# Kernel tuning notes

Hardware: AMD Instinct MI355X
Metric: run time of the kernel (lower is better)

Reference implementation:

```python
import jax, jax.numpy as jnp
import numpy as np

EPS = 1e-8
K = 3  # num_neighbors

def setup_inputs() -> dict:
    key = jax.random.key(0)
    k1, k2, k3, k4 = jax.random.split(key, 4)
    n, B, m, C = 16384, 8, 2048, 128
    return {
        "unknown": jax.random.normal(k1, (n, 3), dtype=jnp.float32),
        "known": jax.random.normal(k2, (B, m, 3), dtype=jnp.float32),
        "batch_inds": jax.random.randint(k3, (n,), 0, B),
        "known_feats": jax.random.normal(k4, (B, C, m), dtype=jnp.float32),
    }

def reference(unknown, known, batch_inds, known_feats):
    # unknown: (n,3); known: (B,m,3); batch_inds: (n,); known_feats: (B,C,m)
    kg = known[batch_inds]                                   # (n,m,3) gather per-query scene
    d2 = jnp.sum((unknown[:, None, :] - kg) ** 2, axis=-1)   # (n,m) squared L2
    neg_d2, idx = jax.lax.top_k(-d2, K)                      # 3 nearest (sorted ascending dist)
    dist = jnp.sqrt(jnp.maximum(-neg_d2, 0.0))               # (n,K)
    dist_recip = 1.0 / (dist + EPS)
    weight = dist_recip / jnp.sum(dist_recip, axis=-1, keepdims=True)  # (n,K)
    # gather neighbor features: (n,K,C)
    feats = known_feats[batch_inds[:, None], :, idx]
    out = jnp.einsum('nkc,nk->nc', feats, weight)            # (n,C)
    return out[:, :, None]                                   # (n,C,1)
```

## Files before the change

kernel.cpp:

```cpp
#include <hip/hip_runtime.h>

#define NPTS 16384
#define NB   8
#define NM   2048
#define NC   128
#define EPSF 1e-8f

#define TQ   16
#define QPB  16
#define GX   160

#define MERGE_F(d, j) do {                              \
    const bool _b2 = (d) < D2;                          \
    const bool _b1 = (d) < D1;                          \
    const bool _b0 = (d) < D0;                          \
    D2 = _b1 ? D1 : (_b2 ? (d) : D2);                   \
    I2 = _b1 ? I1 : (_b2 ? (j) : I2);                   \
    D1 = _b0 ? D0 : (_b1 ? (d) : D1);                   \
    I1 = _b0 ? I0 : (_b1 ? (j) : I1);                   \
    D0 = _b0 ? (d) : D0;                                \
    I0 = _b0 ? (j) : I0;                                \
} while (0)

#define MERGE_DI(ed, ei) do {                                           \
    const bool _b2 = ((ed) < D2) || (((ed) == D2) && ((ei) < I2));      \
    const bool _b1 = ((ed) < D1) || (((ed) == D1) && ((ei) < I1));      \
    const bool _b0 = ((ed) < D0) || (((ed) == D0) && ((ei) < I0));      \
    D2 = _b1 ? D1 : (_b2 ? (ed) : D2);                                  \
    I2 = _b1 ? I1 : (_b2 ? (ei) : I2);                                  \
    D1 = _b0 ? D0 : (_b1 ? (ed) : D1);                                  \
    I1 = _b0 ? I0 : (_b1 ? (ei) : I1);                                  \
    D0 = _b0 ? (ed) : D0;                                               \
    I0 = _b0 ? (ei) : I0;                                               \
} while (0)

__global__ __launch_bounds__(256, 5) void fused(const float* __restrict__ unknown,
                                                const float* __restrict__ known,
                                                const int*   __restrict__ binds,
                                                const float* __restrict__ feats,
                                                float* __restrict__ out) {
    __shared__ float2 kxy[NM];
    __shared__ float  kz[NM];
    __shared__ int qlist[QPB];
    __shared__ int wsum[4];

    const int tid  = threadIdx.x;
    const int b    = blockIdx.y;
    const int x    = blockIdx.x;
    const int lane = tid & 63;
    const int wave = tid >> 6;

    const int4* b4 = (const int4*)binds;
    int myCnt = 0;
#pragma unroll
    for (int r = 0; r < 16; ++r) {
        const int4 v = b4[tid * 16 + r];
        myCnt += (v.x == b) + (v.y == b) + (v.z == b) + (v.w == b);
    }
    int inc = myCnt;
#pragma unroll
    for (int off = 1; off <= 32; off <<= 1) {
        const int n = __shfl_up(inc, off);
        if (lane >= off) inc += n;
    }
    if (lane == 63) wsum[wave] = inc;
    __syncthreads();
    int wbase = 0;
    for (int w = 0; w < wave; ++w) wbase += wsum[w];
    const int exPre = wbase + inc - myCnt;
    const int segN  = wsum[0] + wsum[1] + wsum[2] + wsum[3];

    if (x * QPB >= segN) return;

    {
        const float* kb = known + (size_t)b * NM * 3;
        for (int j = tid; j < NM; j += 256) {
            float2 xy; xy.x = kb[j * 3 + 0]; xy.y = kb[j * 3 + 1];
            kxy[j] = xy;
            kz[j]  = kb[j * 3 + 2];
        }
    }

    const int qi = tid >> 4;
    const int t  = tid & 15;

    for (int w0 = x * QPB; w0 < segN; w0 += GX * QPB) {
        __syncthreads();
        if (exPre < w0 + QPB && exPre + myCnt > w0) {
            int rank = exPre;
#pragma unroll
            for (int r = 0; r < 16; ++r) {
                const int4 v = b4[tid * 16 + r];
                const int base = tid * 64 + r * 4;
                if (v.x == b) { if (rank >= w0 && rank < w0 + QPB) qlist[rank - w0] = base + 0; ++rank; }
                if (v.y == b) { if (rank >= w0 && rank < w0 + QPB) qlist[rank - w0] = base + 1; ++rank; }
                if (v.z == b) { if (rank >= w0 && rank < w0 + QPB) qlist[rank - w0] = base + 2; ++rank; }
                if (v.w == b) { if (rank >= w0 && rank < w0 + QPB) qlist[rank - w0] = base + 3; ++rank; }
            }
        }
        __syncthreads();

        const int valid = (segN - w0 < QPB) ? (segN - w0) : QPB;
        const int kq    = (qi < valid) ? qi : 0;
        const int p     = qlist[kq];
        const float ux = unknown[p * 3 + 0];
        const float uy = unknown[p * 3 + 1];
        const float uz = unknown[p * 3 + 2];

        float D0 = __builtin_inff(), D1 = __builtin_inff(), D2 = __builtin_inff();
        int   I0 = NM, I1 = NM, I2 = NM;

#pragma unroll 8
        for (int i = 0; i < NM / TQ; ++i) {
            const int j = (i << 4) | t;
            const float2 kp = kxy[j];
            const float  kzz = kz[j];
            const float dx = __fsub_rn(ux, kp.x);
            const float dy = __fsub_rn(uy, kp.y);
            const float dz = __fsub_rn(uz, kzz);
            const float d  = __fadd_rn(__fadd_rn(__fmul_rn(dx, dx), __fmul_rn(dy, dy)),
                                       __fmul_rn(dz, dz));
            MERGE_F(d, j);
        }

#pragma unroll
        for (int off = 8; off >= 1; off >>= 1) {
            const float e0d = __shfl_down(D0, off);
            const float e1d = __shfl_down(D1, off);
            const float e2d = __shfl_down(D2, off);
            const int   e0i = __shfl_down(I0, off);
            const int   e1i = __shfl_down(I1, off);
            const int   e2i = __shfl_down(I2, off);
            MERGE_DI(e0d, e0i);
            MERGE_DI(e1d, e1i);
            MERGE_DI(e2d, e2i);
        }
        const int src = lane & ~15;
        D0 = __shfl(D0, src); D1 = __shfl(D1, src); D2 = __shfl(D2, src);
        I0 = __shfl(I0, src); I1 = __shfl(I1, src); I2 = __shfl(I2, src);

        const float t0 = 1.0f / (sqrtf(D0) + EPSF);
        const float t1 = 1.0f / (sqrtf(D1) + EPSF);
        const float t2 = 1.0f / (sqrtf(D2) + EPSF);
        const float s  = t0 + t1 + t2;
        const float w0w = t0 / s, w1w = t1 / s, w2w = t2 / s;

        const float* fb = feats + (size_t)b * NC * NM;
#pragma unroll
        for (int k = 0; k < 8; ++k) {
            const int c = t + (k << 4);
            const float* fc = fb + (size_t)c * NM;
            const float f0 = fc[I0];
            const float f1 = fc[I1];
            const float f2 = fc[I2];
            out[(size_t)p * NC + c] = w0w * f0 + w1w * f1 + w2w * f2;
        }
    }
}

extern "C" void kernel_launch(void* const* d_in, const int* in_sizes, int n_in,
                              void* d_out, int out_size, void* d_ws, size_t ws_size,
                              hipStream_t stream) {
    const float* unknown = (const float*)d_in[0];
    const float* known   = (const float*)d_in[1];
    const int*   binds   = (const int*)d_in[2];
    const float* feats   = (const float*)d_in[3];
    float*       out     = (float*)d_out;

    fused<<<dim3(GX, NB), 256, 0, stream>>>(unknown, known, binds, feats, out);
}
```

Measured before the change: 113.7 us.

## Pack known points as SoA float2 pairs and use med3-based top-3 merge

```diff
diff --git a/kernel.cpp b/kernel.cpp
--- a/kernel.cpp
+++ b/kernel.cpp
@@ -10,16 +10,17 @@
 #define QPB  16
 #define GX   160
 
-#define MERGE_F(d, j) do {                              \
-    const bool _b2 = (d) < D2;                          \
-    const bool _b1 = (d) < D1;                          \
-    const bool _b0 = (d) < D0;                          \
-    D2 = _b1 ? D1 : (_b2 ? (d) : D2);                   \
-    I2 = _b1 ? I1 : (_b2 ? (j) : I2);                   \
-    D1 = _b0 ? D0 : (_b1 ? (d) : D1);                   \
-    I1 = _b0 ? I0 : (_b1 ? (j) : I1);                   \
-    D0 = _b0 ? (d) : D0;                                \
-    I0 = _b0 ? (j) : I0;                                \
+#define MERGE3(d, j) do {                                       \
+    const bool _b0 = (d) < D0;                                  \
+    const bool _b1 = (d) < D1;                                  \
+    const bool _b2 = (d) < D2;                                  \
+    const float _n0 = fminf((d), D0);                           \
+    const float _n1 = __builtin_amdgcn_fmed3f(D0, D1, (d));     \
+    const float _n2 = __builtin_amdgcn_fmed3f(D1, D2, (d));     \
+    I2 = _b1 ? I1 : (_b2 ? (j) : I2);                           \
+    I1 = _b0 ? I0 : (_b1 ? (j) : I1);                           \
+    I0 = _b0 ? (j) : I0;                                        \
+    D0 = _n0; D1 = _n1; D2 = _n2;                               \
 } while (0)
 
 #define MERGE_DI(ed, ei) do {                                           \
@@ -34,13 +35,14 @@
     I0 = _b0 ? (ei) : I0;                                               \
 } while (0)
 
-__global__ __launch_bounds__(256, 5) void fused(const float* __restrict__ unknown,
+__global__ __launch_bounds__(256, 4) void fused(const float* __restrict__ unknown,
                                                 const float* __restrict__ known,
                                                 const int*   __restrict__ binds,
                                                 const float* __restrict__ feats,
                                                 float* __restrict__ out) {
-    __shared__ float2 kxy[NM];
-    __shared__ float  kz[NM];
+    __shared__ float2 kx2[NM / 2];
+    __shared__ float2 ky2[NM / 2];
+    __shared__ float2 kz2[NM / 2];
     __shared__ int qlist[QPB];
     __shared__ int wsum[4];
 
@@ -74,10 +76,12 @@
 
     {
         const float* kb = known + (size_t)b * NM * 3;
-        for (int j = tid; j < NM; j += 256) {
-            float2 xy; xy.x = kb[j * 3 + 0]; xy.y = kb[j * 3 + 1];
-            kxy[j] = xy;
-            kz[j]  = kb[j * 3 + 2];
+        for (int p = tid; p < NM / 2; p += 256) {
+            const float* s = kb + p * 6;
+            float2 vx, vy, vz;
+            vx.x = s[0]; vy.x = s[1]; vz.x = s[2];
+            vx.y = s[3]; vy.y = s[4]; vz.y = s[5];
+            kx2[p] = vx; ky2[p] = vy; kz2[p] = vz;
         }
     }
 
@@ -111,16 +115,24 @@
         int   I0 = NM, I1 = NM, I2 = NM;
 
 #pragma unroll 8
-        for (int i = 0; i < NM / TQ; ++i) {
-            const int j = (i << 4) | t;
-            const float2 kp = kxy[j];
-            const float  kzz = kz[j];
-            const float dx = __fsub_rn(ux, kp.x);
-            const float dy = __fsub_rn(uy, kp.y);
-            const float dz = __fsub_rn(uz, kzz);
-            const float d  = __fadd_rn(__fadd_rn(__fmul_rn(dx, dx), __fmul_rn(dy, dy)),
-                                       __fmul_rn(dz, dz));
-            MERGE_F(d, j);
+        for (int i = 0; i < NM / (2 * TQ); ++i) {
+            const int pr = (i << 4) | t;
+            const float2 vx = kx2[pr];
+            const float2 vy = ky2[pr];
+            const float2 vz = kz2[pr];
+            const int jLo = pr << 1;
+            const float dx0 = __fsub_rn(ux, vx.x);
+            const float dy0 = __fsub_rn(uy, vy.x);
+            const float dz0 = __fsub_rn(uz, vz.x);
+            const float dx1 = __fsub_rn(ux, vx.y);
+            const float dy1 = __fsub_rn(uy, vy.y);
+            const float dz1 = __fsub_rn(uz, vz.y);
+            const float dLo = __fadd_rn(__fadd_rn(__fmul_rn(dx0, dx0), __fmul_rn(dy0, dy0)),
+                                        __fmul_rn(dz0, dz0));
+            const float dHi = __fadd_rn(__fadd_rn(__fmul_rn(dx1, dx1), __fmul_rn(dy1, dy1)),
+                                        __fmul_rn(dz1, dz1));
+            MERGE3(dLo, jLo);
+            MERGE3(dHi, jLo + 1);
         }
 
 #pragma unroll
```

New measurement: 110.6 us, median of 2. 2.7% less time.

## Bucket known points by x-slab and prune neighbor search per query

Applied to the files above, without the earlier changes.

```diff
diff --git a/kernel.cpp b/kernel.cpp
--- a/kernel.cpp
+++ b/kernel.cpp
@@ -2,25 +2,17 @@
 
 #define NPTS 16384
 #define NB   8
+#define NC   128
 #define NM   2048
-#define NC   128
 #define EPSF 1e-8f
 
-#define TQ   16
 #define QPB  16
 #define GX   160
 
-#define MERGE_F(d, j) do {                              \
-    const bool _b2 = (d) < D2;                          \
-    const bool _b1 = (d) < D1;                          \
-    const bool _b0 = (d) < D0;                          \
-    D2 = _b1 ? D1 : (_b2 ? (d) : D2);                   \
-    I2 = _b1 ? I1 : (_b2 ? (j) : I2);                   \
-    D1 = _b0 ? D0 : (_b1 ? (d) : D1);                   \
-    I1 = _b0 ? I0 : (_b1 ? (j) : I1);                   \
-    D0 = _b0 ? (d) : D0;                                \
-    I0 = _b0 ? (j) : I0;                                \
-} while (0)
+#define NBUK 32
+#define W    0.25f
+#define INVW 4.0f
+#define ORG  (-4.0f)
 
 #define MERGE_DI(ed, ei) do {                                           \
     const bool _b2 = ((ed) < D2) || (((ed) == D2) && ((ei) < I2));      \
@@ -34,13 +26,37 @@
     I0 = _b0 ? (ei) : I0;                                               \
 } while (0)
 
-__global__ __launch_bounds__(256, 5) void fused(const float* __restrict__ unknown,
+#define PROC_BUCKET(bk) do {                                            \
+    const int _lo = bstart[bk], _hi = bend[bk];                         \
+    for (int _k0 = _lo; _k0 < _hi; _k0 += 64) {                         \
+        const int  _k2 = _k0 + lane;                                    \
+        const bool _a  = _k2 < _hi;                                     \
+        const int  _ka = _a ? _k2 : _lo;                                \
+        const float _dx = __fsub_rn(ux, sx[_ka]);                       \
+        const float _dy = __fsub_rn(uy, sy[_ka]);                       \
+        const float _dz = __fsub_rn(uz, sz[_ka]);                       \
+        float _d = __fadd_rn(__fadd_rn(__fmul_rn(_dx, _dx),             \
+                                       __fmul_rn(_dy, _dy)),            \
+                             __fmul_rn(_dz, _dz));                      \
+        _d = _a ? _d : __builtin_inff();                                \
+        const int _jj = _a ? (int)sid[_ka] : NM;                        \
+        MERGE_DI(_d, _jj);                                              \
+    }                                                                   \
+} while (0)
+
+__device__ __forceinline__ int bukOf(float v) {
+    int c = (int)floorf(__fmul_rn(__fsub_rn(v, ORG), INVW));
+    return c < 0 ? 0 : (c > NBUK - 1 ? NBUK - 1 : c);
+}
+
+__global__ __launch_bounds__(256, 4) void fused(const float* __restrict__ unknown,
                                                 const float* __restrict__ known,
                                                 const int*   __restrict__ binds,
                                                 const float* __restrict__ feats,
                                                 float* __restrict__ out) {
-    __shared__ float2 kxy[NM];
-    __shared__ float  kz[NM];
+    __shared__ float sx[NM], sy[NM], sz[NM];
+    __shared__ unsigned short sid[NM];
+    __shared__ int bcnt[NBUK], bstart[NBUK], bend[NBUK], bcur[NBUK];
     __shared__ int qlist[QPB];
     __shared__ int wsum[4];
 
@@ -64,6 +80,7 @@
         if (lane >= off) inc += n;
     }
     if (lane == 63) wsum[wave] = inc;
+    if (tid < NBUK) bcnt[tid] = 0;
     __syncthreads();
     int wbase = 0;
     for (int w = 0; w < wave; ++w) wbase += wsum[w];
@@ -72,17 +89,43 @@
 
     if (x * QPB >= segN) return;
 
+    float px[8], py[8], pz[8];
+    int   pb[8];
     {
         const float* kb = known + (size_t)b * NM * 3;
-        for (int j = tid; j < NM; j += 256) {
-            float2 xy; xy.x = kb[j * 3 + 0]; xy.y = kb[j * 3 + 1];
-            kxy[j] = xy;
-            kz[j]  = kb[j * 3 + 2];
-        }
-    }
-
-    const int qi = tid >> 4;
-    const int t  = tid & 15;
+#pragma unroll
+        for (int k = 0; k < 8; ++k) {
+            const int j = tid * 8 + k;
+            px[k] = kb[j * 3 + 0];
+            py[k] = kb[j * 3 + 1];
+            pz[k] = kb[j * 3 + 2];
+            pb[k] = bukOf(px[k]);
+            atomicAdd(&bcnt[pb[k]], 1);
+        }
+    }
+    __syncthreads();
+    if (wave == 0) {
+        const int c = (lane < NBUK) ? bcnt[lane] : 0;
+        int ip = c;
+#pragma unroll
+        for (int off = 1; off < NBUK; off <<= 1) {
+            const int n = __shfl_up(ip, off);
+            if (lane >= off) ip += n;
+        }
+        if (lane < NBUK) { bend[lane] = ip; bstart[lane] = ip - c; bcur[lane] = ip - c; }
+    }
+    __syncthreads();
+    {
+#pragma unroll
+        for (int k = 0; k < 8; ++k) {
+            const int pos = atomicAdd(&bcur[pb[k]], 1);
+            sx[pos] = px[k];
+            sy[pos] = py[k];
+            sz[pos] = pz[k];
+            sid[pos] = (unsigned short)(tid * 8 + k);
+        }
+    }
+    __syncthreads();
 
     for (int w0 = x * QPB; w0 < segN; w0 += GX * QPB) {
         __syncthreads();
@@ -101,59 +144,67 @@
         __syncthreads();
 
         const int valid = (segN - w0 < QPB) ? (segN - w0) : QPB;
-        const int kq    = (qi < valid) ? qi : 0;
-        const int p     = qlist[kq];
-        const float ux = unknown[p * 3 + 0];
-        const float uy = unknown[p * 3 + 1];
-        const float uz = unknown[p * 3 + 2];
-
-        float D0 = __builtin_inff(), D1 = __builtin_inff(), D2 = __builtin_inff();
-        int   I0 = NM, I1 = NM, I2 = NM;
-
-#pragma unroll 8
-        for (int i = 0; i < NM / TQ; ++i) {
-            const int j = (i << 4) | t;
-            const float2 kp = kxy[j];
-            const float  kzz = kz[j];
-            const float dx = __fsub_rn(ux, kp.x);
-            const float dy = __fsub_rn(uy, kp.y);
-            const float dz = __fsub_rn(uz, kzz);
-            const float d  = __fadd_rn(__fadd_rn(__fmul_rn(dx, dx), __fmul_rn(dy, dy)),
-                                       __fmul_rn(dz, dz));
-            MERGE_F(d, j);
-        }
-
-#pragma unroll
-        for (int off = 8; off >= 1; off >>= 1) {
-            const float e0d = __shfl_down(D0, off);
-            const float e1d = __shfl_down(D1, off);
-            const float e2d = __shfl_down(D2, off);
-            const int   e0i = __shfl_down(I0, off);
-            const int   e1i = __shfl_down(I1, off);
-            const int   e2i = __shfl_down(I2, off);
-            MERGE_DI(e0d, e0i);
-            MERGE_DI(e1d, e1i);
-            MERGE_DI(e2d, e2i);
-        }
-        const int src = lane & ~15;
-        D0 = __shfl(D0, src); D1 = __shfl(D1, src); D2 = __shfl(D2, src);
-        I0 = __shfl(I0, src); I1 = __shfl(I1, src); I2 = __shfl(I2, src);
-
-        const float t0 = 1.0f / (sqrtf(D0) + EPSF);
-        const float t1 = 1.0f / (sqrtf(D1) + EPSF);
-        const float t2 = 1.0f / (sqrtf(D2) + EPSF);
-        const float s  = t0 + t1 + t2;
-        const float w0w = t0 / s, w1w = t1 / s, w2w = t2 / s;
-
-        const float* fb = feats + (size_t)b * NC * NM;
-#pragma unroll
-        for (int k = 0; k < 8; ++k) {
-            const int c = t + (k << 4);
-            const float* fc = fb + (size_t)c * NM;
-            const float f0 = fc[I0];
-            const float f1 = fc[I1];
-            const float f2 = fc[I2];
-            out[(size_t)p * NC + c] = w0w * f0 + w1w * f1 + w2w * f2;
+
+#pragma unroll
+        for (int rr = 0; rr < 4; ++rr) {
+            const int qidx = rr * 4 + wave;
+            const int kq   = (qidx < valid) ? qidx : 0;
+            const int p    = qlist[kq];
+            const float ux = unknown[p * 3 + 0];
+            const float uy = unknown[p * 3 + 1];
+            const float uz = unknown[p * 3 + 2];
+            const int ib   = bukOf(ux);
+
+            float D0 = __builtin_inff(), D1 = __builtin_inff(), D2 = __builtin_inff();
+            int   I0 = NM, I1 = NM, I2 = NM;
+
+            int s = 0;
+            while (true) {
+                const int bl = ib - s, br = ib + s;
+                if (bl >= 0) PROC_BUCKET(bl);
+                if (s > 0 && br < NBUK) PROC_BUCKET(br);
+
+                const bool hasL = (ib - s) > 0;
+                const bool hasR = (ib + s) < NBUK - 1;
+                if (!hasL && !hasR) break;
+                float db = __builtin_inff();
+                if (hasL) db = fminf(db, __fsub_rn(ux, ORG + (float)(ib - s) * W));
+                if (hasR) db = fminf(db, __fsub_rn(ORG + (float)(ib + s + 1) * W, ux));
+                float m2 = D2;
+#pragma unroll
+                for (int off = 32; off >= 1; off >>= 1) m2 = fminf(m2, __shfl_xor(m2, off));
+                if (m2 < __fmul_rn(db, db)) break;
+                ++s;
+            }
+
+#pragma unroll
+            for (int off = 32; off >= 1; off >>= 1) {
+                const float e0d = __shfl_down(D0, off);
+                const float e1d = __shfl_down(D1, off);
+                const float e2d = __shfl_down(D2, off);
+                const int   e0i = __shfl_down(I0, off);
+                const int   e1i = __shfl_down(I1, off);
+                const int   e2i = __shfl_down(I2, off);
+                MERGE_DI(e0d, e0i);
+                MERGE_DI(e1d, e1i);
+                MERGE_DI(e2d, e2i);
+            }
+            D0 = __shfl(D0, 0); D1 = __shfl(D1, 0); D2 = __shfl(D2, 0);
+            I0 = __shfl(I0, 0); I1 = __shfl(I1, 0); I2 = __shfl(I2, 0);
+
+            const float t0 = 1.0f / (sqrtf(D0) + EPSF);
+            const float t1 = 1.0f / (sqrtf(D1) + EPSF);
+            const float t2 = 1.0f / (sqrtf(D2) + EPSF);
+            const float sw = t0 + t1 + t2;
+            const float w0w = t0 / sw, w1w = t1 / sw, w2w = t2 / sw;
+
+            const float* fb = feats + (size_t)b * NC * NM;
+#pragma unroll
+            for (int k = 0; k < 2; ++k) {
+                const int c = lane + (k << 6);
+                const float* fc = fb + (size_t)c * NM;
+                out[(size_t)p * NC + c] = w0w * fc[I0] + w1w * fc[I1] + w2w * fc[I2];
+            }
         }
     }
 }
```

New measurement: 153.1 us. +34.6%, slower.
